# Optimization experiments

Hardware: AMD Instinct MI355X
Metric: run time of the kernel (lower is better)

The kernel has to match this reference:

```python
import jax, jax.numpy as jnp
import numpy as np

D_MODEL = 768
N_HEAD = 12
D_FF = 3072
EPS = 1e-5


def _layer_norm(x, w, b):
    mu = jnp.mean(x, axis=-1, keepdims=True)
    var = jnp.mean(jnp.square(x - mu), axis=-1, keepdims=True)
    return (x - mu) * jax.lax.rsqrt(var + EPS) * w + b


def setup_inputs() -> dict:
    key = jax.random.key(0)
    ks = jax.random.split(key, 8)
    B, S, D = 2, 4096, D_MODEL
    s_in = 1.0 / np.sqrt(D)
    s_ff = 1.0 / np.sqrt(D_FF)
    return {
        "src": jax.random.normal(ks[0], (B, S, D), jnp.float32),
        "w_qkv": jax.random.uniform(ks[1], (3 * D, D), jnp.float32, -s_in, s_in),
        "b_qkv": jnp.zeros((3 * D,), jnp.float32),
        "w_out": jax.random.uniform(ks[2], (D, D), jnp.float32, -s_in, s_in),
        "b_out": jnp.zeros((D,), jnp.float32),
        "w1": jax.random.uniform(ks[3], (D_FF, D), jnp.float32, -s_in, s_in),
        "b1": jnp.zeros((D_FF,), jnp.float32),
        "w2": jax.random.uniform(ks[4], (D, D_FF), jnp.float32, -s_ff, s_ff),
        "b2": jnp.zeros((D,), jnp.float32),
        "ln1_w": jnp.ones((D,), jnp.float32),
        "ln1_b": jnp.zeros((D,), jnp.float32),
        "ln2_w": jnp.ones((D,), jnp.float32),
        "ln2_b": jnp.zeros((D,), jnp.float32),
    }


def reference(src, w_qkv, b_qkv, w_out, b_out, w1, b1, w2, b2,
              ln1_w, ln1_b, ln2_w, ln2_b):
    B, S, D = src.shape
    H, dh = N_HEAD, D // N_HEAD
    # fused QKV projection: [B,S,3D]
    qkv = jnp.einsum('bsd,ed->bse', src, w_qkv) + b_qkv
    q, k, v = jnp.split(qkv, 3, axis=-1)
    q = q.reshape(B, S, H, dh)
    k = k.reshape(B, S, H, dh)
    v = v.reshape(B, S, H, dh)
    scale = 1.0 / np.sqrt(dh)
    scores = jnp.einsum('bqhd,bkhd->bhqk', q, k) * scale  # [B,H,S,S]
    attn = jax.nn.softmax(scores, axis=-1)
    ctx = jnp.einsum('bhqk,bkhd->bqhd', attn, v).reshape(B, S, D)
    attn_out = jnp.einsum('bsd,ed->bse', ctx, w_out) + b_out
    # post-norm residual (norm_first=False), dropout inactive in eval
    x = _layer_norm(src + attn_out, ln1_w, ln1_b)
    h = jax.nn.relu(jnp.einsum('bsd,fd->bsf', x, w1) + b1)
    ffn = jnp.einsum('bsf,df->bsd', h, w2) + b2
    return _layer_norm(x + ffn, ln2_w, ln2_b)
```

## Files before the change

### kernel.cpp

```cpp
#include <hip/hip_runtime.h>
#include <hip/hip_bf16.h>

typedef __hip_bfloat16 bf16;
typedef __attribute__((ext_vector_type(8))) short s16x8;
typedef __attribute__((ext_vector_type(4))) float f32x4;

#define MFMA16x16x32(A, B, C) __builtin_amdgcn_mfma_f32_16x16x32_bf16((A), (B), (C), 0, 0, 0)

__device__ __forceinline__ void async_copy16(const bf16* g, bf16* l) {
  __builtin_amdgcn_global_load_lds(
      (const __attribute__((address_space(1))) void*)g,
      (__attribute__((address_space(3))) void*)l, 16, 0, 0);
}

__device__ __forceinline__ int SW(int row, int chunk) {
  return row * 64 + (((chunk) ^ (row & 7)) << 3);
}

__global__ __launch_bounds__(256)
void cast_all_kernel(const float* __restrict__ s0, bf16* __restrict__ d0,
                     const float* __restrict__ s1, bf16* __restrict__ d1,
                     const float* __restrict__ s2, bf16* __restrict__ d2,
                     const float* __restrict__ s3, bf16* __restrict__ d3,
                     const float* __restrict__ s4, bf16* __restrict__ d4) {
  int blk = blockIdx.x;
  const float* in; bf16* out;
  if (blk < 1728)      { in = s0; out = d0; }
  else if (blk < 2304) { in = s1; out = d1; blk -= 1728; }
  else if (blk < 4608) { in = s2; out = d2; blk -= 2304; }
  else if (blk < 6912) { in = s3; out = d3; blk -= 4608; }
  else                 { in = s4; out = d4; blk -= 6912; }
  const int i = (blk * 256 + threadIdx.x) * 4;
  const float4 f = *(const float4*)(in + i);
  out[i + 0] = (bf16)f.x; out[i + 1] = (bf16)f.y;
  out[i + 2] = (bf16)f.z; out[i + 3] = (bf16)f.w;
}

template <int RELU, int VT, int ACCUM, int CN, typename OutT>
__global__ __launch_bounds__(256)
void gemm_bt_kernel(const bf16* __restrict__ A, const bf16* __restrict__ B,
                    const float* __restrict__ bias, OutT* __restrict__ C,
                    int N, int K, int lda, int ldb, bf16* __restrict__ C2) {
  constexpr int NJ = CN / 32;
  __shared__ __align__(16) bf16 As[2][128 * 32];
  __shared__ __align__(16) bf16 Bs[2][CN * 32];

  const int t = threadIdx.x;
  const int lane = t & 63;
  const int wave = t >> 6;
  const int wm = (wave >> 1) << 6;
  const int wn = (wave & 1) * (CN / 2);
  const int col16 = lane & 15;
  const int quad = lane >> 4;
  const int bm = blockIdx.x;
  const int bn = blockIdx.y;

  const bf16* Ag = A + (size_t)(bm * 128 + (t >> 2)) * lda + (t & 3) * 8;
  const bf16* Bg = B + (size_t)(bn * CN + (t >> 2)) * ldb + (t & 3) * 8;

  f32x4 acc[4][NJ] = {};

  async_copy16(Ag, &As[0][0] + t * 8);
  async_copy16(Ag + (size_t)64 * lda, &As[0][0] + 2048 + t * 8);
  async_copy16(Bg, &Bs[0][0] + t * 8);
  if (CN == 128)
    async_copy16(Bg + (size_t)64 * ldb, &Bs[0][0] + 2048 + t * 8);

  int n = 0;
  for (int k0 = 0; k0 < K; k0 += 32, n ^= 1) {
    __syncthreads();
    if (k0 + 32 < K) {
      const int k1 = k0 + 32;
      async_copy16(Ag + k1, &As[n ^ 1][0] + t * 8);
      async_copy16(Ag + (size_t)64 * lda + k1, &As[n ^ 1][0] + 2048 + t * 8);
      async_copy16(Bg + k1, &Bs[n ^ 1][0] + t * 8);
      if (CN == 128)
        async_copy16(Bg + (size_t)64 * ldb + k1, &Bs[n ^ 1][0] + 2048 + t * 8);
    }
    const bf16* asn = &As[n][0];
    const bf16* bsn = &Bs[n][0];

    s16x8 af[4], bfr[NJ];
#pragma unroll
    for (int i = 0; i < 4; i++)
      af[i] = *(const s16x8*)(asn + (wm + i * 16 + col16) * 32 + quad * 8);
#pragma unroll
    for (int j = 0; j < NJ; j++)
      bfr[j] = *(const s16x8*)(bsn + (wn + j * 16 + col16) * 32 + quad * 8);
#pragma unroll
    for (int i = 0; i < 4; i++)
#pragma unroll
      for (int j = 0; j < NJ; j++)
        acc[i][j] = MFMA16x16x32(af[i], bfr[j], acc[i][j]);
  }

  const int row0 = bm * 128 + wm + quad * 4;
  const int col0 = bn * CN + wn + col16;
#pragma unroll
  for (int j = 0; j < NJ; j++) {
    const int col = col0 + j * 16;
    const float bv = ACCUM ? 0.0f : bias[col];
#pragma unroll
    for (int i = 0; i < 4; i++) {
#pragma unroll
      for (int r = 0; r < 4; r++) {
        float v = acc[i][j][r] + bv;
        if (RELU) v = fmaxf(v, 0.0f);
        const int row = row0 + i * 16 + r;
        if (VT == 2) {
          if (col < 1536) {
            C[(size_t)row * N + col] = (OutT)v;
          } else {
            const int cc = col - 1536;
            C2[(size_t)((row >> 12) * 12 + (cc >> 6)) * 262144 +
               (cc & 63) * 4096 + (row & 4095)] = (bf16)v;
          }
        } else {
          const size_t idx = (size_t)row * N + col;
          if (ACCUM) v += ((const float*)C)[idx];
          C[idx] = (OutT)v;
        }
      }
    }
  }
}

__global__ __launch_bounds__(256)
void attn_kernel(const bf16* __restrict__ QK, const bf16* __restrict__ Vt,
                 bf16* __restrict__ Opart, float* __restrict__ lbuf) {
  __shared__ __align__(16) bf16 pool[22528];

  const int t = threadIdx.x, lane = t & 63, wave = t >> 6;
  const int col16 = lane & 15, quad = lane >> 4;
  const int b = blockIdx.z, h = blockIdx.y;
  const int ks = blockIdx.x >> 4;
  const int qblk = blockIdx.x & 15;
  const int qw0 = qblk * 256 + wave * 64;

  s16x8 bq[4][2];
#pragma unroll
  for (int qt = 0; qt < 4; qt++)
#pragma unroll
    for (int s = 0; s < 2; s++) {
      union { s16x8 v; bf16 hh[8]; } u;
      u.v = *(const s16x8*)(QK + (size_t)(b * 4096 + qw0 + qt * 16 + col16) * 1536 +
                            h * 64 + s * 32 + quad * 8);
#pragma unroll
      for (int e = 0; e < 8; e++) u.hh[e] = (bf16)((float)u.hh[e] * 0.18033688f);
      bq[qt][s] = u.v;
    }

  union { s16x8 v; short s_[8]; } uo1;
#pragma unroll
  for (int e = 0; e < 8; e++) uo1.s_[e] = (short)0x3F80;
  const s16x8 aones = uo1.v;

  const int krow = t >> 3;
  const int kch = (t & 7) ^ (krow & 7);
  const int vrow = t >> 2;
  const int vch = (t & 3) ^ ((vrow >> 1) & 3);
  const bf16* kgb = QK + (size_t)(b * 4096) * 1536 + 768 + h * 64;
  const bf16* vgb = Vt + (size_t)(b * 12 + h) * 262144;
  const bf16* ksrc = kgb + (size_t)krow * 1536 + kch * 8;
  const bf16* vsrc = vgb + (size_t)vrow * 4096 + vch * 8;

  f32x4 o[4][4] = {};
  f32x4 lacc[4] = {};
  bf16* pw = pool + 12288 + wave * 2560;

  const int kbeg = ks * 2048, kend = kbeg + 2048;

  async_copy16(ksrc + (size_t)kbeg * 1536, pool + t * 8);
  async_copy16(vsrc + kbeg, pool + 6144 + t * 8);
  async_copy16(ksrc + (size_t)(kbeg + 32) * 1536, pool + 2048 + t * 8);
  async_copy16(vsrc + kbeg + 32, pool + 6144 + 2048 + t * 8);

  int ib = 0;
  for (int k0 = kbeg; k0 < kend; k0 += 32) {
    const int ip = (ib + 2 >= 3) ? ib - 1 : ib + 2;
    if (k0 + 64 < kend) {
      async_copy16(ksrc + (size_t)(k0 + 64) * 1536, pool + ip * 2048 + t * 8);
      async_copy16(vsrc + k0 + 64, pool + 6144 + ip * 2048 + t * 8);
      asm volatile("s_waitcnt vmcnt(4)" ::: "memory");
    } else if (k0 + 32 < kend) {
      asm volatile("s_waitcnt vmcnt(2)" ::: "memory");
    } else {
      asm volatile("s_waitcnt vmcnt(0)" ::: "memory");
    }
    __builtin_amdgcn_s_barrier();
    __builtin_amdgcn_sched_barrier(0);

    const bf16* ksn = pool + ib * 2048;
    const bf16* vsn = pool + 6144 + ib * 2048;

    s16x8 ak[2][2];
#pragma unroll
    for (int s = 0; s < 2; s++)
#pragma unroll
      for (int kt = 0; kt < 2; kt++)
        ak[s][kt] = *(const s16x8*)(ksn + SW(kt * 16 + col16, s * 4 + quad));

#pragma unroll
    for (int kt = 0; kt < 2; kt++) {
      f32x4 st[4] = {};
#pragma unroll
      for (int s = 0; s < 2; s++)
#pragma unroll
        for (int qt = 0; qt < 4; qt++)
          st[qt] = MFMA16x16x32(ak[s][kt], bq[qt][s], st[qt]);
#pragma unroll
      for (int qt = 0; qt < 4; qt++) {
        union { unsigned long long u; bf16 hh[4]; } pk;
#pragma unroll
        for (int r = 0; r < 4; r++)
          pk.hh[r] = (bf16)__builtin_amdgcn_exp2f(st[qt][r]);
        *(unsigned long long*)(pw + (qt * 16 + col16) * 40 + kt * 16 + quad * 4) =
            pk.u;
      }
    }
    asm volatile("s_waitcnt lgkmcnt(0)" ::: "memory");

    s16x8 bp[4];
#pragma unroll
    for (int qt = 0; qt < 4; qt++)
      bp[qt] = *(const s16x8*)(pw + (qt * 16 + col16) * 40 + quad * 8);
#pragma unroll
    for (int qt = 0; qt < 4; qt++)
      lacc[qt] = MFMA16x16x32(aones, bp[qt], lacc[qt]);
#pragma unroll
    for (int dt = 0; dt < 4; dt++) {
      const int vr = dt * 16 + col16;
      const s16x8 av = *(const s16x8*)(vsn + vr * 32 +
                                       ((quad ^ ((vr >> 1) & 3)) << 3));
#pragma unroll
      for (int qt = 0; qt < 4; qt++)
        o[dt][qt] = MFMA16x16x32(av, bp[qt], o[dt][qt]);
    }

    ib = (ib + 1 == 3) ? 0 : ib + 1;
  }

  if (lane < 16) {
#pragma unroll
    for (int qt = 0; qt < 4; qt++)
      lbuf[(size_t)ks * 98304 + (size_t)(b * 4096 + qw0 + qt * 16 + lane) * 12 + h] =
          lacc[qt][0];
  }

  __syncthreads();
  bf16* ep = pool + wave * 4096;
#pragma unroll
  for (int qt = 0; qt < 4; qt++)
#pragma unroll
    for (int dt = 0; dt < 4; dt++)
#pragma unroll
      for (int r = 0; r < 4; r++)
        ep[(qt * 16 + col16) * 64 + (((dt * 2 + (quad >> 1)) ^ (col16 & 7)) << 3) +
           (quad & 1) * 4 + r] = (bf16)(o[dt][qt][r]);
  asm volatile("s_waitcnt lgkmcnt(0)" ::: "memory");
  const int qrow = lane >> 1, chalf = (lane & 1) * 4;
#pragma unroll
  for (int h2 = 0; h2 < 2; h2++) {
    const int rl = h2 * 32 + qrow;
    bf16* dst = Opart + (size_t)ks * 6291456 +
                (size_t)(b * 4096 + qw0 + rl) * 768 + h * 64 + chalf * 8;
#pragma unroll
    for (int i = 0; i < 4; i++)
      *(s16x8*)(dst + i * 8) = *(const s16x8*)(ep + SW(rl, chalf + i));
  }
}

__global__ __launch_bounds__(256)
void attn_combine_kernel(const bf16* __restrict__ Opart,
                         const float* __restrict__ lbuf,
                         bf16* __restrict__ ctx) {
  const int i = blockIdx.x * 256 + threadIdx.x;
  const int row = i / 96, c8 = i % 96;
  const int h = c8 >> 3;
  const float inv = 1.0f / (lbuf[(size_t)row * 12 + h] +
                            lbuf[98304 + (size_t)row * 12 + h]);
  union { s16x8 v; bf16 hh[8]; } ua, ub, uo;
  ua.v = *(const s16x8*)(Opart + (size_t)row * 768 + c8 * 8);
  ub.v = *(const s16x8*)(Opart + 6291456 + (size_t)row * 768 + c8 * 8);
#pragma unroll
  for (int j = 0; j < 8; j++)
    uo.hh[j] = (bf16)(((float)ua.hh[j] + (float)ub.hh[j]) * inv);
  *(s16x8*)(ctx + (size_t)row * 768 + c8 * 8) = uo.v;
}

__global__ __launch_bounds__(256)
void add_ln_b_kernel(const float* __restrict__ X, const float* __restrict__ Y,
                     const float* __restrict__ w, const float* __restrict__ b,
                     bf16* __restrict__ out) {
  const int row = blockIdx.x * 4 + (threadIdx.x >> 6);
  const int lane = threadIdx.x & 63;
  const float* x = X + (size_t)row * 768;
  const float* y = Y + (size_t)row * 768;
  float v[12];
  float s = 0.0f;
#pragma unroll
  for (int i = 0; i < 3; i++) {
    const int c = lane * 4 + i * 256;
    const float4 xf = *(const float4*)(x + c);
    const float4 yf = *(const float4*)(y + c);
    v[i * 4 + 0] = xf.x + yf.x; v[i * 4 + 1] = xf.y + yf.y;
    v[i * 4 + 2] = xf.z + yf.z; v[i * 4 + 3] = xf.w + yf.w;
    s += v[i * 4] + v[i * 4 + 1] + v[i * 4 + 2] + v[i * 4 + 3];
  }
#pragma unroll
  for (int off = 32; off > 0; off >>= 1) s += __shfl_xor(s, off, 64);
  const float mu = s * (1.0f / 768.0f);
  float var = 0.0f;
#pragma unroll
  for (int i = 0; i < 12; i++) { const float d = v[i] - mu; var += d * d; }
#pragma unroll
  for (int off = 32; off > 0; off >>= 1) var += __shfl_xor(var, off, 64);
  const float rs = rsqrtf(var * (1.0f / 768.0f) + 1e-5f);
#pragma unroll
  for (int i = 0; i < 12; i++) {
    const int c = lane * 4 + (i >> 2) * 256 + (i & 3);
    out[(size_t)row * 768 + c] = (bf16)((v[i] - mu) * rs * w[c] + b[c]);
  }
}

__global__ __launch_bounds__(256)
void add_ln_f_kernel(const bf16* __restrict__ X, const float* __restrict__ Y,
                     const float* __restrict__ w, const float* __restrict__ b,
                     float* __restrict__ out) {
  const int row = blockIdx.x * 4 + (threadIdx.x >> 6);
  const int lane = threadIdx.x & 63;
  const bf16* x = X + (size_t)row * 768;
  const float* y = Y + (size_t)row * 768;
  float v[12];
  float s = 0.0f;
#pragma unroll
  for (int i = 0; i < 3; i++) {
    const int c = lane * 4 + i * 256;
    const float4 yf = *(const float4*)(y + c);
    v[i * 4 + 0] = (float)x[c + 0] + yf.x; v[i * 4 + 1] = (float)x[c + 1] + yf.y;
    v[i * 4 + 2] = (float)x[c + 2] + yf.z; v[i * 4 + 3] = (float)x[c + 3] + yf.w;
    s += v[i * 4] + v[i * 4 + 1] + v[i * 4 + 2] + v[i * 4 + 3];
  }
#pragma unroll
  for (int off = 32; off > 0; off >>= 1) s += __shfl_xor(s, off, 64);
  const float mu = s * (1.0f / 768.0f);
  float var = 0.0f;
#pragma unroll
  for (int i = 0; i < 12; i++) { const float d = v[i] - mu; var += d * d; }
#pragma unroll
  for (int off = 32; off > 0; off >>= 1) var += __shfl_xor(var, off, 64);
  const float rs = rsqrtf(var * (1.0f / 768.0f) + 1e-5f);
#pragma unroll
  for (int i = 0; i < 12; i++) {
    const int c = lane * 4 + (i >> 2) * 256 + (i & 3);
    out[(size_t)row * 768 + c] = (v[i] - mu) * rs * w[c] + b[c];
  }
}

extern "C" void kernel_launch(void* const* d_in, const int* in_sizes, int n_in,
                              void* d_out, int out_size, void* d_ws, size_t ws_size,
                              hipStream_t stream) {
  (void)in_sizes; (void)n_in; (void)out_size; (void)ws_size;
  const float* src   = (const float*)d_in[0];
  const float* w_qkv = (const float*)d_in[1];
  const float* b_qkv = (const float*)d_in[2];
  const float* w_out = (const float*)d_in[3];
  const float* b_out = (const float*)d_in[4];
  const float* w1    = (const float*)d_in[5];
  const float* b1    = (const float*)d_in[6];
  const float* w2    = (const float*)d_in[7];
  const float* b2    = (const float*)d_in[8];
  const float* ln1w  = (const float*)d_in[9];
  const float* ln1b  = (const float*)d_in[10];
  const float* ln2w  = (const float*)d_in[11];
  const float* ln2b  = (const float*)d_in[12];
  float* out = (float*)d_out;

  char* ws = (char*)d_ws;
  bf16* wqkvb = (bf16*)ws;
  bf16* woutb = (bf16*)(ws + 3538944);
  bf16* w1b   = (bf16*)(ws + 4718592);
  bf16* w2b   = (bf16*)(ws + 9437184);
  bf16* srcb  = (bf16*)(ws + 14155776);
  bf16* QK    = (bf16*)(ws + 26738688);
  bf16* Vt    = (bf16*)(ws + 51904512);
  bf16* Opart = (bf16*)d_out;
  float* lbuf = (float*)ws;
  bf16* ctx   = (bf16*)(ws + 14155776);
  float* attn_out = (float*)(ws + 26738688);
  bf16* x1b   = (bf16*)(ws + 51904512);
  bf16* hbuf  = (bf16*)(ws + 14155776);
  float* ffn  = out;

  cast_all_kernel<<<13056, 256, 0, stream>>>(
      w_qkv, wqkvb, w_out, woutb, w1, w1b, w2, w2b, src, srcb);

  gemm_bt_kernel<0, 2, 0, 128, bf16><<<dim3(64, 18), 256, 0, stream>>>(
      srcb, wqkvb, b_qkv, QK, 1536, 768, 768, 768, Vt);
  attn_kernel<<<dim3(32, 12, 2), 256, 0, stream>>>(QK, Vt, Opart, lbuf);
  attn_combine_kernel<<<3072, 256, 0, stream>>>(Opart, lbuf, ctx);
  gemm_bt_kernel<0, 0, 0, 64, float><<<dim3(64, 12), 256, 0, stream>>>(
      ctx, woutb, b_out, attn_out, 768, 768, 768, 768, nullptr);
  add_ln_b_kernel<<<2048, 256, 0, stream>>>(src, attn_out, ln1w, ln1b, x1b);
  for (int c = 0; c < 2; c++) {
    gemm_bt_kernel<1, 0, 0, 128, bf16><<<dim3(64, 12), 256, 0, stream>>>(
        x1b, w1b + (size_t)c * 1536 * 768, b1 + c * 1536, hbuf, 1536, 768, 768,
        768, nullptr);
    if (c == 0)
      gemm_bt_kernel<0, 0, 0, 64, float><<<dim3(64, 12), 256, 0, stream>>>(
          hbuf, w2b + c * 1536, b2, ffn, 768, 1536, 1536, 3072, nullptr);
    else
      gemm_bt_kernel<0, 0, 1, 64, float><<<dim3(64, 12), 256, 0, stream>>>(
          hbuf, w2b + c * 1536, b2, ffn, 768, 1536, 1536, 3072, nullptr);
  }
  add_ln_f_kernel<<<2048, 256, 0, stream>>>(x1b, ffn, ln2w, ln2b, out);
}
```

Baseline: 470.1 us.

## Shrink attention LDS to double buffering, remap block order, raise occupancy hint

Reduces the attention kernel's shared memory by switching from a three-stage to a two-stage K/V ring and removing padding from the per-wave probability buffer. It adds a launch_bounds occupancy hint and remaps the block index so consecutive blocks cover different heads, aiming for better L2 locality. V swizzle is changed to match. The risk is that the shallower prefetch exposes load latency behind a full barrier each step, and that the unpadded P buffer causes LDS bank conflicts.

```diff
diff --git a/kernel.cpp b/kernel.cpp
--- a/kernel.cpp
+++ b/kernel.cpp
@@ -125,16 +125,20 @@
   }
 }
 
-__global__ __launch_bounds__(256)
+__global__ __launch_bounds__(256, 3)
 void attn_kernel(const bf16* __restrict__ QK, const bf16* __restrict__ Vt,
                  bf16* __restrict__ Opart, float* __restrict__ lbuf) {
-  __shared__ __align__(16) bf16 pool[22528];
+  __shared__ __align__(16) bf16 pool[16384];
 
   const int t = threadIdx.x, lane = t & 63, wave = t >> 6;
   const int col16 = lane & 15, quad = lane >> 4;
-  const int b = blockIdx.z, h = blockIdx.y;
-  const int ks = blockIdx.x >> 4;
-  const int qblk = blockIdx.x & 15;
+
+  const int w = blockIdx.x + 32 * (blockIdx.y + 12 * blockIdx.z);
+  const int g = (w & 7) + 8 * ((w >> 3) >> 5);
+  const int x = (w >> 3) & 31;
+  const int b = g / 12, h = g % 12;
+  const int ks = x >> 4;
+  const int qblk = x & 15;
   const int qw0 = qblk * 256 + wave * 64;
 
   s16x8 bq[4][2];
@@ -158,7 +162,7 @@
   const int krow = t >> 3;
   const int kch = (t & 7) ^ (krow & 7);
   const int vrow = t >> 2;
-  const int vch = (t & 3) ^ ((vrow >> 1) & 3);
+  const int vch = (t & 3) ^ (vrow & 3);
   const bf16* kgb = QK + (size_t)(b * 4096) * 1536 + 768 + h * 64;
   const bf16* vgb = Vt + (size_t)(b * 12 + h) * 262144;
   const bf16* ksrc = kgb + (size_t)krow * 1536 + kch * 8;
@@ -166,32 +170,22 @@
 
   f32x4 o[4][4] = {};
   f32x4 lacc[4] = {};
-  bf16* pw = pool + 12288 + wave * 2560;
+  bf16* pw = pool + 8192 + wave * 2048;
 
   const int kbeg = ks * 2048, kend = kbeg + 2048;
 
   async_copy16(ksrc + (size_t)kbeg * 1536, pool + t * 8);
-  async_copy16(vsrc + kbeg, pool + 6144 + t * 8);
-  async_copy16(ksrc + (size_t)(kbeg + 32) * 1536, pool + 2048 + t * 8);
-  async_copy16(vsrc + kbeg + 32, pool + 6144 + 2048 + t * 8);
-
-  int ib = 0;
-  for (int k0 = kbeg; k0 < kend; k0 += 32) {
-    const int ip = (ib + 2 >= 3) ? ib - 1 : ib + 2;
-    if (k0 + 64 < kend) {
-      async_copy16(ksrc + (size_t)(k0 + 64) * 1536, pool + ip * 2048 + t * 8);
-      async_copy16(vsrc + k0 + 64, pool + 6144 + ip * 2048 + t * 8);
-      asm volatile("s_waitcnt vmcnt(4)" ::: "memory");
-    } else if (k0 + 32 < kend) {
-      asm volatile("s_waitcnt vmcnt(2)" ::: "memory");
-    } else {
-      asm volatile("s_waitcnt vmcnt(0)" ::: "memory");
-    }
-    __builtin_amdgcn_s_barrier();
-    __builtin_amdgcn_sched_barrier(0);
-
-    const bf16* ksn = pool + ib * 2048;
-    const bf16* vsn = pool + 6144 + ib * 2048;
+  async_copy16(vsrc + kbeg, pool + 4096 + t * 8);
+
+  int n = 0;
+  for (int k0 = kbeg; k0 < kend; k0 += 32, n ^= 1) {
+    __syncthreads();
+    if (k0 + 32 < kend) {
+      async_copy16(ksrc + (size_t)(k0 + 32) * 1536, pool + (n ^ 1) * 2048 + t * 8);
+      async_copy16(vsrc + (k0 + 32), pool + 4096 + (n ^ 1) * 2048 + t * 8);
+    }
+    const bf16* ksn = pool + n * 2048;
+    const bf16* vsn = pool + 4096 + n * 2048;
 
     s16x8 ak[2][2];
 #pragma unroll
@@ -214,7 +208,7 @@
 #pragma unroll
         for (int r = 0; r < 4; r++)
           pk.hh[r] = (bf16)__builtin_amdgcn_exp2f(st[qt][r]);
-        *(unsigned long long*)(pw + (qt * 16 + col16) * 40 + kt * 16 + quad * 4) =
+        *(unsigned long long*)(pw + (qt * 16 + col16) * 32 + kt * 16 + quad * 4) =
             pk.u;
       }
     }
@@ -223,21 +217,18 @@
     s16x8 bp[4];
 #pragma unroll
     for (int qt = 0; qt < 4; qt++)
-      bp[qt] = *(const s16x8*)(pw + (qt * 16 + col16) * 40 + quad * 8);
+      bp[qt] = *(const s16x8*)(pw + (qt * 16 + col16) * 32 + quad * 8);
 #pragma unroll
     for (int qt = 0; qt < 4; qt++)
       lacc[qt] = MFMA16x16x32(aones, bp[qt], lacc[qt]);
 #pragma unroll
     for (int dt = 0; dt < 4; dt++) {
       const int vr = dt * 16 + col16;
-      const s16x8 av = *(const s16x8*)(vsn + vr * 32 +
-                                       ((quad ^ ((vr >> 1) & 3)) << 3));
+      const s16x8 av = *(const s16x8*)(vsn + vr * 32 + ((quad ^ (vr & 3)) << 3));
 #pragma unroll
       for (int qt = 0; qt < 4; qt++)
         o[dt][qt] = MFMA16x16x32(av, bp[qt], o[dt][qt]);
     }
-
-    ib = (ib + 1 == 3) ? 0 : ib + 1;
   }
 
   if (lane < 16) {
```

Result: slower. 501.5 us (+6.7%).
